# Performance work log

Measured on AMD Instinct MI355X. Metric: run time of the kernel, lower is better.

The kernel has to match this reference:

```python
import jax, jax.numpy as jnp
import numpy as np

XYZ, DIRS, APP = 63, 27, 0
HID, OUT, NLAYERS, SKIPS = 256, 4, 8, (4,)

def _linear_init(key, fan_in, fan_out):
    kw, kb = jax.random.split(key)
    s = 1.0 / np.sqrt(fan_in)
    W = jax.random.uniform(kw, (fan_in, fan_out), jnp.float32, -s, s)
    b = jax.random.uniform(kb, (fan_out,), jnp.float32, -s, s)
    return W, b

def setup_inputs() -> dict:
    key = jax.random.key(0)
    keys = jax.random.split(key, NLAYERS + 2)
    x = jax.random.normal(keys[0], (262144, XYZ + DIRS + APP), jnp.float32)
    d = {"x": x}
    in_dim = XYZ
    for i in range(NLAYERS):
        # skip-concat: layer after a skip index sees hid+xyz inputs
        fan_in = HID + XYZ if (i - 1) in SKIPS else (XYZ if i == 0 else HID)
        W, b = _linear_init(keys[i + 1], fan_in, HID)
        d[f"W{i}"], d[f"b{i}"] = W, b
    Wout, bout = _linear_init(keys[-1], HID, OUT)
    d["Wout"], d["bout"] = Wout, bout
    return d

def reference(x, W0, b0, W1, b1, W2, b2, W3, b3, W4, b4, W5, b5, W6, b6, W7, b7, Wout, bout):
    Ws = [W0, W1, W2, W3, W4, W5, W6, W7]
    bs = [b0, b1, b2, b3, b4, b5, b6, b7]
    input_pts = x[..., :XYZ]  # dirs/app split off but unused (use_viewdirs=False)
    h = input_pts
    for i in range(NLAYERS):
        h = jax.nn.relu(h @ Ws[i] + bs[i])
        if i in SKIPS:
            h = jnp.concatenate([input_pts, h], axis=-1)
    return h @ Wout + bout  # [N, 4] = rgb + density logits
```

## Files before the change

### kernel.cpp

```cpp
#include <hip/hip_runtime.h>


typedef _Float16 h8 __attribute__((ext_vector_type(8)));
typedef float f4 __attribute__((ext_vector_type(4)));

#define OFF_L0   0
#define OFF_L1   16384
#define OFF_L2   81920
#define OFF_L3   147456
#define OFF_L4   212992
#define OFF_L5   278528
#define OFF_L6   360448
#define OFF_L7   425984
#define OFF_OUT  491520
#define TOT_HALVES 495616
#define TOT_GROUPS (TOT_HALVES / 8)

__global__ void nerf_prep(const float* __restrict__ W0, const float* __restrict__ W1,
                          const float* __restrict__ W2, const float* __restrict__ W3,
                          const float* __restrict__ W4, const float* __restrict__ W5,
                          const float* __restrict__ W6, const float* __restrict__ W7,
                          const float* __restrict__ Wout, _Float16* __restrict__ wf)
{
    int g = blockIdx.x * 256 + threadIdx.x;
    if (g >= TOT_GROUPS) return;

    const int bounds[10] = {0, 2048, 10240, 18432, 26624, 34816, 45056, 53248, 61440, 61952};
    const float* Ws[9] = {W0, W1, W2, W3, W4, W5, W6, W7, Wout};

    int L = 0;
    while (L < 8 && g >= bounds[L + 1]) ++L;

    int t    = g - bounds[L];
    int lane = t & 63;
    int q    = t >> 6;
    int NF   = (L == 8) ? 1 : 16;
    int nf   = q % NF;
    int ks   = q / NF;
    int n    = nf * 16 + (lane & 15);
    int k0   = ks * 32 + (lane >> 4) * 8;

    const float* W = Ws[L];
    h8 v;
#pragma unroll
    for (int i = 0; i < 8; ++i) {
        int k = k0 + i;
        float val = 0.f;
        if (L == 0) {
            if (k < 63) val = W[k * 256 + n];
        } else if (L == 5) {
            if (k < 256)            val = W[(63 + k) * 256 + n];
            else if ((k - 256) < 63) val = W[(k - 256) * 256 + n];
        } else if (L == 8) {
            if (n < 4) val = W[k * 4 + n];
        } else {
            val = W[k * 256 + n];
        }
        v[i] = (_Float16)val;
    }
    *(h8*)(wf + (size_t)g * 8) = v;
}

template <int KSTEPS, int MODE>
__device__ __forceinline__ void mlp_layer(_Float16 (&hbuf)[64][264], _Float16 (&xbuf)[64][72],
                                          const _Float16* __restrict__ wfrag,
                                          const float* __restrict__ bias,
                                          int wid, int lane)
{
    const int lg = lane >> 4, ln = lane & 15;

    f4 acc[4][4];
#pragma unroll
    for (int mf = 0; mf < 4; ++mf)
#pragma unroll
        for (int nf = 0; nf < 4; ++nf)
#pragma unroll
            for (int i = 0; i < 4; ++i) acc[mf][nf][i] = 0.f;

#pragma unroll
    for (int ks = 0; ks < KSTEPS; ++ks) {
        h8 bfr[4];
#pragma unroll
        for (int nf = 0; nf < 4; ++nf)
            bfr[nf] = *(const h8*)(wfrag + (size_t)((ks * 16 + (wid * 4 + nf)) * 64 + lane) * 8);

#pragma unroll
        for (int mf = 0; mf < 4; ++mf) {
            const _Float16* ap;
            if constexpr (MODE == 1) {
                ap = &xbuf[mf * 16 + ln][ks * 32 + lg * 8];
            } else if constexpr (MODE == 2) {
                ap = (ks < 8) ? &hbuf[mf * 16 + ln][ks * 32 + lg * 8]
                              : &xbuf[mf * 16 + ln][(ks - 8) * 32 + lg * 8];
            } else {
                ap = &hbuf[mf * 16 + ln][ks * 32 + lg * 8];
            }
            h8 afr = *(const h8*)ap;
#pragma unroll
            for (int nf = 0; nf < 4; ++nf)
                acc[mf][nf] = __builtin_amdgcn_mfma_f32_16x16x32_f16(afr, bfr[nf], acc[mf][nf], 0, 0, 0);
        }
    }

    __syncthreads();

#pragma unroll
    for (int nf = 0; nf < 4; ++nf) {
        float bv = bias[wid * 64 + nf * 16 + ln];
#pragma unroll
        for (int mf = 0; mf < 4; ++mf) {
#pragma unroll
            for (int i = 0; i < 4; ++i) {
                float v = acc[mf][nf][i] + bv;
                v = fmaxf(v, 0.f);
                hbuf[mf * 16 + lg * 4 + i][wid * 64 + nf * 16 + ln] = (_Float16)v;
            }
        }
    }
    __syncthreads();
}

__global__ __launch_bounds__(256, 2) void nerf_fused(
    const float* __restrict__ x,
    const float* __restrict__ b0, const float* __restrict__ b1, const float* __restrict__ b2,
    const float* __restrict__ b3, const float* __restrict__ b4, const float* __restrict__ b5,
    const float* __restrict__ b6, const float* __restrict__ b7, const float* __restrict__ bout,
    const _Float16* __restrict__ wf,
    float* __restrict__ out)
{
    __shared__ _Float16 hbuf[64][264];
    __shared__ _Float16 xbuf[64][72];

    const int tid  = threadIdx.x;
    const int wid  = tid >> 6;
    const int lane = tid & 63;
    const int lg   = lane >> 4, ln = lane & 15;
    const int row0 = blockIdx.x * 64;

    for (int idx = tid; idx < 64 * 64; idx += 256) {
        int r = idx >> 6, c = idx & 63;
        float v = (c < 63) ? x[(size_t)(row0 + r) * 90 + c] : 0.f;
        xbuf[r][c] = (_Float16)v;
    }
    __syncthreads();

    mlp_layer<2, 1>(hbuf, xbuf, wf + OFF_L0, b0, wid, lane);
    mlp_layer<8, 0>(hbuf, xbuf, wf + OFF_L1, b1, wid, lane);
    mlp_layer<8, 0>(hbuf, xbuf, wf + OFF_L2, b2, wid, lane);
    mlp_layer<8, 0>(hbuf, xbuf, wf + OFF_L3, b3, wid, lane);
    mlp_layer<8, 0>(hbuf, xbuf, wf + OFF_L4, b4, wid, lane);
    mlp_layer<10, 2>(hbuf, xbuf, wf + OFF_L5, b5, wid, lane);
    mlp_layer<8, 0>(hbuf, xbuf, wf + OFF_L6, b6, wid, lane);
    mlp_layer<8, 0>(hbuf, xbuf, wf + OFF_L7, b7, wid, lane);

    f4 oacc;
#pragma unroll
    for (int i = 0; i < 4; ++i) oacc[i] = 0.f;
#pragma unroll
    for (int ks = 0; ks < 8; ++ks) {
        h8 bfr = *(const h8*)(wf + OFF_OUT + (size_t)(ks * 64 + lane) * 8);
        h8 afr = *(const h8*)&hbuf[wid * 16 + ln][ks * 32 + lg * 8];
        oacc = __builtin_amdgcn_mfma_f32_16x16x32_f16(afr, bfr, oacc, 0, 0, 0);
    }
    if (ln < 4) {
        float bo = bout[ln];
#pragma unroll
        for (int i = 0; i < 4; ++i) {
            int r = row0 + wid * 16 + lg * 4 + i;
            out[(size_t)r * 4 + ln] = oacc[i] + bo;
        }
    }
}

extern "C" void kernel_launch(void* const* d_in, const int* in_sizes, int n_in,
                              void* d_out, int out_size, void* d_ws, size_t ws_size,
                              hipStream_t stream)
{
    const float* x = (const float*)d_in[0];
    const float* W[9];
    const float* b[9];
    for (int i = 0; i < 8; ++i) {
        W[i] = (const float*)d_in[1 + 2 * i];
        b[i] = (const float*)d_in[2 + 2 * i];
    }
    W[8] = (const float*)d_in[17];
    b[8] = (const float*)d_in[18];

    _Float16* wf = (_Float16*)d_ws;

    nerf_prep<<<(TOT_GROUPS + 255) / 256, 256, 0, stream>>>(
        W[0], W[1], W[2], W[3], W[4], W[5], W[6], W[7], W[8], wf);

    nerf_fused<<<262144 / 64, 256, 0, stream>>>(
        x, b[0], b[1], b[2], b[3], b[4], b[5], b[6], b[7], b[8], wf,
        (float*)d_out);
}
```

Before: 259.3 us.

## Double-buffer weight fragments in registers across k-steps and layers

Weight B-fragments are now prefetched two k-steps ahead into a register double buffer, and the last two steps of each layer prefetch the first fragments of the next layer, so global/L2 weight loads overlap with MFMA work. Bias loads are hoisted to the start of each layer. The launch bound is raised from 2 to 3 blocks per CU, which tightens the register budget while prefetch adds 32 extra VGPRs and may cause spills.

```diff
diff --git a/kernel.cpp b/kernel.cpp
--- a/kernel.cpp
+++ b/kernel.cpp
@@ -61,14 +61,25 @@
     *(h8*)(wf + (size_t)g * 8) = v;
 }
 
-template <int KSTEPS, int MODE>
+__device__ __forceinline__ const h8* bfrag_ptr(const _Float16* __restrict__ w,
+                                               int ks, int wid, int nf, int lane)
+{
+    return (const h8*)(w + (size_t)((ks * 16 + (wid * 4 + nf)) * 64 + lane) * 8);
+}
+
+template <int KSTEPS, int MODE, bool LAST>
 __device__ __forceinline__ void mlp_layer(_Float16 (&hbuf)[64][264], _Float16 (&xbuf)[64][72],
                                           const _Float16* __restrict__ wfrag,
+                                          const _Float16* __restrict__ wnext,
                                           const float* __restrict__ bias,
-                                          int wid, int lane)
+                                          int wid, int lane, h8 (&pf)[2][4])
 {
     const int lg = lane >> 4, ln = lane & 15;
 
+    float bv[4];
+#pragma unroll
+    for (int nf = 0; nf < 4; ++nf) bv[nf] = bias[wid * 64 + nf * 16 + ln];
+
     f4 acc[4][4];
 #pragma unroll
     for (int mf = 0; mf < 4; ++mf)
@@ -79,11 +90,6 @@
 
 #pragma unroll
     for (int ks = 0; ks < KSTEPS; ++ks) {
-        h8 bfr[4];
-#pragma unroll
-        for (int nf = 0; nf < 4; ++nf)
-            bfr[nf] = *(const h8*)(wfrag + (size_t)((ks * 16 + (wid * 4 + nf)) * 64 + lane) * 8);
-
 #pragma unroll
         for (int mf = 0; mf < 4; ++mf) {
             const _Float16* ap;
@@ -98,7 +104,16 @@
             h8 afr = *(const h8*)ap;
 #pragma unroll
             for (int nf = 0; nf < 4; ++nf)
-                acc[mf][nf] = __builtin_amdgcn_mfma_f32_16x16x32_f16(afr, bfr[nf], acc[mf][nf], 0, 0, 0);
+                acc[mf][nf] = __builtin_amdgcn_mfma_f32_16x16x32_f16(afr, pf[ks & 1][nf], acc[mf][nf], 0, 0, 0);
+        }
+        if (ks + 2 < KSTEPS) {
+#pragma unroll
+            for (int nf = 0; nf < 4; ++nf)
+                pf[ks & 1][nf] = *bfrag_ptr(wfrag, ks + 2, wid, nf, lane);
+        } else if constexpr (!LAST) {
+#pragma unroll
+            for (int nf = 0; nf < 4; ++nf)
+                pf[ks & 1][nf] = *bfrag_ptr(wnext, ks + 2 - KSTEPS, wid, nf, lane);
         }
     }
 
@@ -106,12 +121,11 @@
 
 #pragma unroll
     for (int nf = 0; nf < 4; ++nf) {
-        float bv = bias[wid * 64 + nf * 16 + ln];
 #pragma unroll
         for (int mf = 0; mf < 4; ++mf) {
 #pragma unroll
             for (int i = 0; i < 4; ++i) {
-                float v = acc[mf][nf][i] + bv;
+                float v = acc[mf][nf][i] + bv[nf];
                 v = fmaxf(v, 0.f);
                 hbuf[mf * 16 + lg * 4 + i][wid * 64 + nf * 16 + ln] = (_Float16)v;
             }
@@ -120,7 +134,7 @@
     __syncthreads();
 }
 
-__global__ __launch_bounds__(256, 2) void nerf_fused(
+__global__ __launch_bounds__(256, 3) void nerf_fused(
     const float* __restrict__ x,
     const float* __restrict__ b0, const float* __restrict__ b1, const float* __restrict__ b2,
     const float* __restrict__ b3, const float* __restrict__ b4, const float* __restrict__ b5,
@@ -137,6 +151,13 @@
     const int lg   = lane >> 4, ln = lane & 15;
     const int row0 = blockIdx.x * 64;
 
+    h8 pf[2][4];
+#pragma unroll
+    for (int s = 0; s < 2; ++s)
+#pragma unroll
+        for (int nf = 0; nf < 4; ++nf)
+            pf[s][nf] = *bfrag_ptr(wf + OFF_L0, s, wid, nf, lane);
+
     for (int idx = tid; idx < 64 * 64; idx += 256) {
         int r = idx >> 6, c = idx & 63;
         float v = (c < 63) ? x[(size_t)(row0 + r) * 90 + c] : 0.f;
@@ -144,14 +165,14 @@
     }
     __syncthreads();
 
-    mlp_layer<2, 1>(hbuf, xbuf, wf + OFF_L0, b0, wid, lane);
-    mlp_layer<8, 0>(hbuf, xbuf, wf + OFF_L1, b1, wid, lane);
-    mlp_layer<8, 0>(hbuf, xbuf, wf + OFF_L2, b2, wid, lane);
-    mlp_layer<8, 0>(hbuf, xbuf, wf + OFF_L3, b3, wid, lane);
-    mlp_layer<8, 0>(hbuf, xbuf, wf + OFF_L4, b4, wid, lane);
-    mlp_layer<10, 2>(hbuf, xbuf, wf + OFF_L5, b5, wid, lane);
-    mlp_layer<8, 0>(hbuf, xbuf, wf + OFF_L6, b6, wid, lane);
-    mlp_layer<8, 0>(hbuf, xbuf, wf + OFF_L7, b7, wid, lane);
+    mlp_layer<2, 1, false>(hbuf, xbuf, wf + OFF_L0, wf + OFF_L1, b0, wid, lane, pf);
+    mlp_layer<8, 0, false>(hbuf, xbuf, wf + OFF_L1, wf + OFF_L2, b1, wid, lane, pf);
+    mlp_layer<8, 0, false>(hbuf, xbuf, wf + OFF_L2, wf + OFF_L3, b2, wid, lane, pf);
+    mlp_layer<8, 0, false>(hbuf, xbuf, wf + OFF_L3, wf + OFF_L4, b3, wid, lane, pf);
+    mlp_layer<8, 0, false>(hbuf, xbuf, wf + OFF_L4, wf + OFF_L5, b4, wid, lane, pf);
+    mlp_layer<10, 2, false>(hbuf, xbuf, wf + OFF_L5, wf + OFF_L6, b5, wid, lane, pf);
+    mlp_layer<8, 0, false>(hbuf, xbuf, wf + OFF_L6, wf + OFF_L7, b6, wid, lane, pf);
+    mlp_layer<8, 0, true>(hbuf, xbuf, wf + OFF_L7, wf + OFF_L7, b7, wid, lane, pf);
 
     f4 oacc;
 #pragma unroll
```

Result: faster. 238.0 us (-8.2%).
